# Optimization experiments

Measured on AMD Instinct MI355X. Metric: run time of the kernel, lower is better.

Reference implementation:

```python
import jax, jax.numpy as jnp
import numpy as np

N, T, D_MODEL, H, DK = 4, 4096, 1024, 16, 64


def setup_inputs() -> dict:
    key = jax.random.key(0)
    ks = jax.random.split(key, 16)
    randn = lambda k, sh: jax.random.normal(k, sh, dtype=jnp.float32)
    # linear weights stored (in, out) so y = x @ W + b (math-equivalent to torch Linear)
    scale = 1.0 / np.sqrt(D_MODEL)
    return {
        "x_k": randn(ks[0], (N, T, D_MODEL)),
        "x_v": randn(ks[1], (N, T, D_MODEL)),
        "x_q": randn(ks[2], (N, T, D_MODEL)),
        "mask": jnp.ones((N, T), dtype=jnp.int32),
        "Wk": randn(ks[3], (D_MODEL, H * DK)) * scale,
        "bk": randn(ks[4], (H * DK,)) * 0.02,
        "Wv": randn(ks[5], (D_MODEL, H * DK)) * scale,
        "bv": randn(ks[6], (H * DK,)) * 0.02,
        "Wq": randn(ks[7], (D_MODEL, H * DK)) * scale,
        "bq": randn(ks[8], (H * DK,)) * 0.02,
        "alpha_w": randn(ks[9], (DK,)),
        "beta_w": randn(ks[10], (DK,)),
        "Wr": randn(ks[11], (DK, DK)) * (1.0 / np.sqrt(DK)),
        "br": randn(ks[12], (DK,)) * 0.02,
        "Wfc": randn(ks[13], (H * DK, D_MODEL)) * scale,
        "bfc": randn(ks[14], (D_MODEL,)) * 0.02,
    }


def _split_heads(x):  # (n, t, h*d) -> (n, h, t, d)
    n, t, _ = x.shape
    return x.reshape(n, t, H, DK).transpose(0, 2, 1, 3)


def reference(x_k, x_v, x_q, mask, Wk, bk, Wv, bv, Wq, bq,
              alpha_w, beta_w, Wr, br, Wfc, bfc):
    scale = DK ** (-0.5)
    k = _split_heads(x_k @ Wk + bk)  # (n, h, t, d)
    v = _split_heads(x_v @ Wv + bv)
    q = _split_heads(x_q @ Wq + bq)

    m = (mask == 0)[:, None, :]  # (n, 1, t) True where masked
    neg_inf = jnp.finfo(q.dtype).min

    # alpha pooling over queries -> global query (n, h, d)
    alpha = jnp.einsum('nhtd,d->nht', q, alpha_w) * scale
    alpha = jnp.where(m, neg_inf, alpha)
    alpha = jax.nn.softmax(alpha, axis=-1)
    global_query = jnp.einsum('nht,nhtd->nhd', alpha, q)

    # p = broadcast(global_query) * k, then beta pooling -> global key
    p = global_query[:, :, None, :] * k  # (n, h, t, d)
    beta = jnp.einsum('nhtd,d->nht', p, beta_w) * scale
    beta = jnp.where(m, neg_inf, beta)
    beta = jax.nn.softmax(beta, axis=-1)
    global_key = jnp.einsum('nht,nhtd->nhd', beta, p)

    u = global_key[:, :, None, :] * v  # (n, h, t, d)
    u_r = u @ Wr + br
    A = u_r + q  # (n, h, t, d)
    A = A.transpose(0, 2, 1, 3).reshape(N, T, H * DK)
    return A @ Wfc + bfc
```

## Files before the change

### kernel.cpp

```cpp
#include <hip/hip_runtime.h>

typedef __bf16 bf16x8 __attribute__((ext_vector_type(8)));
typedef float f32x4 __attribute__((ext_vector_type(4)));
typedef unsigned int u32x4 __attribute__((ext_vector_type(4)));
typedef unsigned short u16x4 __attribute__((ext_vector_type(4)));
typedef unsigned short u16x8 __attribute__((ext_vector_type(8)));

#define SEQ_T 4096
#define DMODEL 1024
#define HEADS 16
#define DKH 64
#define MTOK 16384

#define AS1 __attribute__((address_space(1)))
#define AS3 __attribute__((address_space(3)))

__device__ __forceinline__ unsigned short f2bf(float f) {
  unsigned u = __builtin_bit_cast(unsigned int, f);
  u += 0x7FFFu + ((u >> 16) & 1u);
  return (unsigned short)(u >> 16);
}
__device__ __forceinline__ float bf2f(unsigned short h) {
  unsigned u = ((unsigned)h) << 16;
  return __builtin_bit_cast(float, u);
}
__device__ __forceinline__ void gload16(const unsigned short* g, unsigned short* l) {
  __builtin_amdgcn_global_load_lds((const AS1 unsigned int*)(g),
                                   (AS3 unsigned int*)(l), 16, 0, 0);
}

__device__ __forceinline__ void cvt_block(const float* __restrict__ x,
                                          unsigned short* __restrict__ y,
                                          size_t b, int tid) {
  f32x4 a0 = *(const f32x4*)(x + b + tid * 4);
  f32x4 a1 = *(const f32x4*)(x + b + 1024 + tid * 4);
  u16x4 o0, o1;
#pragma unroll
  for (int j = 0; j < 4; ++j) {
    o0[j] = f2bf(a0[j]);
    o1[j] = f2bf(a1[j]);
  }
  *(u16x4*)(y + b + tid * 4) = o0;
  *(u16x4*)(y + b + 1024 + tid * 4) = o1;
}

__global__ void __launch_bounds__(256) k_cvt(const float* __restrict__ x,
                                             unsigned short* __restrict__ y) {
  cvt_block(x, y, (size_t)blockIdx.x * 2048, threadIdx.x);
}

__global__ void __launch_bounds__(256) k_cvt3(const float* __restrict__ xq,
                                              const float* __restrict__ xk,
                                              const float* __restrict__ xv,
                                              unsigned short* __restrict__ oq,
                                              unsigned short* __restrict__ ok,
                                              unsigned short* __restrict__ ov) {
  const int which = blockIdx.x >> 13;
  const float* x = which == 0 ? xq : (which == 1 ? xk : xv);
  unsigned short* y = which == 0 ? oq : (which == 1 ? ok : ov);
  cvt_block(x, y, (size_t)(blockIdx.x & 8191) * 2048, threadIdx.x);
}

__global__ void __launch_bounds__(256) k_wtrans(const float* __restrict__ W,
                                                unsigned short* __restrict__ Wt,
                                                int K, int N) {
  __shared__ float tile[32][33];
  int bn = blockIdx.x * 32, bk = blockIdx.y * 32;
  int tx = threadIdx.x, ty = threadIdx.y;
#pragma unroll
  for (int j = 0; j < 32; j += 8)
    tile[ty + j][tx] = W[(size_t)(bk + ty + j) * N + bn + tx];
  __syncthreads();
#pragma unroll
  for (int j = 0; j < 32; j += 8)
    Wt[(size_t)(bn + ty + j) * K + bk + tx] = f2bf(tile[tx][ty + j]);
}

#define BM 128
#define BN 128
#define BK 64

template <int OBF, int SCORE, int FUSEA>
__global__ void __launch_bounds__(256, 2)
k_gemm(const unsigned short* __restrict__ A, const unsigned short* __restrict__ Bt,
       const float* __restrict__ bias, void* __restrict__ C,
       const int* __restrict__ mask, const float* __restrict__ swt,
       float* __restrict__ sbuf, const unsigned short* __restrict__ qadd,
       int M, int N, int K) {
  __shared__ unsigned short As[BM * BK];
  __shared__ unsigned short Bs[BN * BK];
  const int tid = threadIdx.x;
  const int lane = tid & 63, wid = tid >> 6;
  const int wr = wid >> 1, wc = wid & 1;
  const int l15 = lane & 15, l4 = lane >> 4;

  const int nwg = gridDim.x * gridDim.y;
  const int flat = blockIdx.x + blockIdx.y * gridDim.x;
  const int rm = (flat & 7) * (nwg >> 3) + (flat >> 3);
  const int bx = rm % gridDim.x, by = rm / gridDim.x;
  const int bm = by * BM, bn = bx * BN;

  const unsigned short* Btn = FUSEA ? Bt + ((size_t)(bm >> 12) << 20) : Bt;
  const float* biasn = FUSEA ? bias + ((bm >> 12) << 10) : bias;

  f32x4 acc[4][4];
#pragma unroll
  for (int i = 0; i < 4; ++i)
#pragma unroll
    for (int j = 0; j < 4; ++j)
#pragma unroll
      for (int e = 0; e < 4; ++e) acc[i][j][e] = 0.f;

  const int sgr = lane >> 3;
  const int sgc = (lane & 7) ^ sgr;

  for (int kt = 0; kt < K; kt += BK) {
    __syncthreads();
#pragma unroll
    for (int j = 0; j < 4; ++j) {
      int rb = wid * 32 + j * 8;
      gload16(A + (size_t)(bm + rb + sgr) * K + kt + sgc * 8, As + rb * BK);
    }
#pragma unroll
    for (int j = 0; j < 4; ++j) {
      int rb = wid * 32 + j * 8;
      gload16(Btn + (size_t)(bn + rb + sgr) * K + kt + sgc * 8, Bs + rb * BK);
    }
    __syncthreads();
#pragma unroll
    for (int kh = 0; kh < 2; ++kh) {
      bf16x8 af[4], bfr[4];
#pragma unroll
      for (int m = 0; m < 4; ++m) {
        int ra = wr * 64 + m * 16 + l15;
        int sl = (kh * 4 + l4) ^ (ra & 7);
        af[m] = *(const bf16x8*)(As + ra * BK + sl * 8);
      }
#pragma unroll
      for (int n = 0; n < 4; ++n) {
        int rb = wc * 64 + n * 16 + l15;
        int sl = (kh * 4 + l4) ^ (rb & 7);
        bfr[n] = *(const bf16x8*)(Bs + rb * BK + sl * 8);
      }
#pragma unroll
      for (int m = 0; m < 4; ++m)
#pragma unroll
        for (int n = 0; n < 4; ++n)
          acc[m][n] = __builtin_amdgcn_mfma_f32_16x16x32_bf16(af[m], bfr[n],
                                                              acc[m][n], 0, 0, 0);
    }
  }

  const int crow = bm + wr * 64 + l4 * 4;
  const int ccol = bn + wc * 64 + l15;

  float pacc[4][4];
  const float* wrow = nullptr;
  if (SCORE == 1) wrow = swt;
  if (SCORE) {
#pragma unroll
    for (int m = 0; m < 4; ++m)
#pragma unroll
      for (int e = 0; e < 4; ++e) pacc[m][e] = 0.f;
  }

#pragma unroll
  for (int m = 0; m < 4; ++m)
#pragma unroll
    for (int n = 0; n < 4; ++n) {
      int c = ccol + n * 16;
      float bj = biasn[c];
      float wg = SCORE ? wrow[n * 16 + l15] : 0.f;
#pragma unroll
      for (int e = 0; e < 4; ++e) {
        int r = crow + m * 16 + e;
        float v = acc[m][n][e] + bj;
        if (FUSEA) v += bf2f(qadd[(size_t)r * N + c]);
        if (SCORE) pacc[m][e] += v * wg;
        if (OBF)
          ((unsigned short*)C)[(size_t)r * N + c] = f2bf(v);
        else
          ((float*)C)[(size_t)r * N + c] = v;
      }
    }

  if (SCORE) {
#pragma unroll
    for (int m = 0; m < 4; ++m)
#pragma unroll
      for (int e = 0; e < 4; ++e) {
        float p = pacc[m][e];
        p += __shfl_xor(p, 1);
        p += __shfl_xor(p, 2);
        p += __shfl_xor(p, 4);
        p += __shfl_xor(p, 8);
        if (l15 == 0) {
          int r = crow + m * 16 + e;
          int t = r & (SEQ_T - 1), n = r >> 12;
          float sc = p * 0.125f;
          if (mask[n * SEQ_T + t] == 0) sc = -3.0e38f;
          sbuf[((size_t)n * HEADS + bx * 2 + wc) * SEQ_T + t] = sc;
        }
      }
  }
}

__global__ void __launch_bounds__(256) k_softmax(const float* __restrict__ s,
                                                 float* __restrict__ mxo,
                                                 float* __restrict__ invo) {
  __shared__ float red[4];
  const int tid = threadIdx.x, lane = tid & 63, wid = tid >> 6;
  const float* sb = s + (size_t)blockIdx.x * SEQ_T;
  float m = -3.4e38f;
  for (int t = tid; t < SEQ_T; t += 256) m = fmaxf(m, sb[t]);
#pragma unroll
  for (int o = 1; o < 64; o <<= 1) m = fmaxf(m, __shfl_xor(m, o));
  if (lane == 0) red[wid] = m;
  __syncthreads();
  m = fmaxf(fmaxf(red[0], red[1]), fmaxf(red[2], red[3]));
  __syncthreads();
  float sum = 0.f;
  for (int t = tid; t < SEQ_T; t += 256) sum += __expf(sb[t] - m);
#pragma unroll
  for (int o = 1; o < 64; o <<= 1) sum += __shfl_xor(sum, o);
  if (lane == 0) red[wid] = sum;
  __syncthreads();
  if (tid == 0) {
    mxo[blockIdx.x] = m;
    invo[blockIdx.x] = 1.f / (red[0] + red[1] + red[2] + red[3]);
  }
}

__global__ void __launch_bounds__(256) k_wsum(const unsigned short* __restrict__ X,
                                              const float* __restrict__ s,
                                              const float* __restrict__ mxv,
                                              const float* __restrict__ invv,
                                              float* __restrict__ pbuf) {
  __shared__ float part[16][64];
  const int nh = blockIdx.x >> 4, chunk = blockIdx.x & 15;
  const int n = nh >> 4, h = nh & 15;
  const int tid = threadIdx.x, lane = tid & 63, wid = tid >> 6;
  const int tsub = lane >> 4, dl = lane & 15;
  const float mx = mxv[nh], inv = invv[nh];
  const float* sb = s + (size_t)nh * SEQ_T + chunk * 256;
  const size_t base = ((size_t)n * SEQ_T + chunk * 256) * DMODEL + h * DKH + dl * 4;
  f32x4 acc = {0.f, 0.f, 0.f, 0.f};
  for (int t = wid * 4 + tsub; t < 256; t += 16) {
    float w = __expf(sb[t] - mx) * inv;
    u16x4 xv = *(const u16x4*)(X + base + (size_t)t * DMODEL);
    acc[0] += w * bf2f(xv[0]);
    acc[1] += w * bf2f(xv[1]);
    acc[2] += w * bf2f(xv[2]);
    acc[3] += w * bf2f(xv[3]);
  }
  int g = wid * 4 + tsub;
#pragma unroll
  for (int e = 0; e < 4; ++e) part[g][dl * 4 + e] = acc[e];
  __syncthreads();
  if (tid < 64) {
    float v = 0.f;
#pragma unroll
    for (int gg = 0; gg < 16; ++gg) v += part[gg][tid];
    pbuf[(size_t)blockIdx.x * 64 + tid] = v;
  }
}

__global__ void __launch_bounds__(256) k_wksb(const float* __restrict__ Wk,
                                              const float* __restrict__ bk,
                                              const float* __restrict__ pbuf,
                                              const float* __restrict__ bw,
                                              float* __restrict__ gq,
                                              unsigned short* __restrict__ WksT,
                                              float* __restrict__ bks) {
  const int nh = blockIdx.x, tid = threadIdx.x;
  const int n = nh >> 4, h = nh & 15;
  __shared__ float wvs[64];
  if (tid < 64) {
    float v = 0.f;
#pragma unroll
    for (int c = 0; c < 16; ++c) v += pbuf[((size_t)nh * 16 + c) * 64 + tid];
    gq[(size_t)nh * 64 + tid] = v;
    wvs[tid] = v * bw[tid];
  }
  __syncthreads();
  int c0 = tid * 4;
  u16x4 o;
#pragma unroll
  for (int i = 0; i < 4; ++i) {
    int c = c0 + i;
    const float* wr = Wk + (size_t)c * DMODEL + h * DKH;
    float acc = 0.f;
#pragma unroll
    for (int dd = 0; dd < 64; dd += 4) {
      f32x4 w4 = *(const f32x4*)(wr + dd);
      acc += w4[0] * wvs[dd] + w4[1] * wvs[dd + 1] + w4[2] * wvs[dd + 2] +
             w4[3] * wvs[dd + 3];
    }
    o[i] = f2bf(acc);
  }
  *(u16x4*)(WksT + (size_t)n * 16 * DMODEL + (size_t)h * DMODEL + c0) = o;
  if (tid < 64) {
    float p = bk[h * 64 + tid] * wvs[tid];
#pragma unroll
    for (int ofs = 1; ofs < 64; ofs <<= 1) p += __shfl_xor(p, ofs);
    if (tid == 0) bks[nh] = p;
  }
}

__global__ void __launch_bounds__(128) k_score(const unsigned short* __restrict__ xk,
                                               const unsigned short* __restrict__ WksT,
                                               const float* __restrict__ bks,
                                               const int* __restrict__ mask,
                                               float* __restrict__ sbuf) {
  __shared__ unsigned short Xs[64 * 32];
  __shared__ unsigned short Ws[16 * 32];
  const int tid = threadIdx.x, lane = tid & 63, wid = tid >> 6;
  const int l15 = lane & 15, l4 = lane >> 4;
  const int bm = blockIdx.x * 64;
  const int n = bm >> 12;
  const unsigned short* Wn = WksT + (size_t)n * 16 * DMODEL;

  f32x4 acc[2];
#pragma unroll
  for (int m = 0; m < 2; ++m)
#pragma unroll
    for (int e = 0; e < 4; ++e) acc[m][e] = 0.f;

  const int srow = lane >> 2, scol = (lane & 3) * 8;
  for (int kt = 0; kt < DMODEL; kt += 32) {
    __syncthreads();
#pragma unroll
    for (int j = 0; j < 2; ++j) {
      int rb = wid * 32 + j * 16;
      gload16(xk + (size_t)(bm + rb + srow) * DMODEL + kt + scol, Xs + rb * 32);
    }
    if (wid == 0) gload16(Wn + (size_t)srow * DMODEL + kt + scol, Ws);
    __syncthreads();
    bf16x8 bfr = *(const bf16x8*)(Ws + l15 * 32 + l4 * 8);
#pragma unroll
    for (int m = 0; m < 2; ++m) {
      bf16x8 af = *(const bf16x8*)(Xs + (wid * 32 + m * 16 + l15) * 32 + l4 * 8);
      acc[m] = __builtin_amdgcn_mfma_f32_16x16x32_bf16(af, bfr, acc[m], 0, 0, 0);
    }
  }
  const int h = l15;
  const float bh = bks[n * 16 + h];
#pragma unroll
  for (int m = 0; m < 2; ++m)
#pragma unroll
    for (int e = 0; e < 4; ++e) {
      int r = bm + wid * 32 + m * 16 + l4 * 4 + e;
      int t = r & (SEQ_T - 1);
      float sc = (acc[m][e] + bh) * 0.125f;
      if (mask[n * SEQ_T + t] == 0) sc = -3.0e38f;
      sbuf[((size_t)n * HEADS + h) * SEQ_T + t] = sc;
    }
}

__global__ void __launch_bounds__(256) k_bwsum(const unsigned short* __restrict__ xk,
                                               const float* __restrict__ s,
                                               const float* __restrict__ smx,
                                               const float* __restrict__ sinv,
                                               float* __restrict__ part) {
  __shared__ float eb[16][64];
  const int tc = blockIdx.x, n = blockIdx.y, tid = threadIdx.x;
#pragma unroll
  for (int i = 0; i < 4; ++i) {
    int idx = i * 256 + tid;
    int h = idx >> 6, t = idx & 63;
    int nh = n * 16 + h;
    eb[h][t] = __expf(s[(size_t)nh * SEQ_T + tc * 64 + t] - smx[nh]) * sinv[nh];
  }
  __syncthreads();
  const int c0 = tid * 4;
  f32x4 acc[16];
#pragma unroll
  for (int h = 0; h < 16; ++h)
#pragma unroll
    for (int e = 0; e < 4; ++e) acc[h][e] = 0.f;
  const unsigned short* xb = xk + ((size_t)n * SEQ_T + tc * 64) * DMODEL + c0;
  for (int t = 0; t < 64; ++t) {
    u16x4 xr = *(const u16x4*)(xb + (size_t)t * DMODEL);
    float x0 = bf2f(xr[0]), x1 = bf2f(xr[1]), x2 = bf2f(xr[2]), x3 = bf2f(xr[3]);
#pragma unroll
    for (int h = 0; h < 16; ++h) {
      float w = eb[h][t];
      acc[h][0] += w * x0;
      acc[h][1] += w * x1;
      acc[h][2] += w * x2;
      acc[h][3] += w * x3;
    }
  }
#pragma unroll
  for (int h = 0; h < 16; ++h)
    *(f32x4*)(part + (((size_t)(n * 64 + tc)) * 16 + h) * DMODEL + c0) = acc[h];
}

__global__ void __launch_bounds__(256) k_gkrw(const float* __restrict__ part,
                                              const unsigned short* __restrict__ WkT,
                                              const float* __restrict__ bk,
                                              const float* __restrict__ gq,
                                              const float* __restrict__ Wr,
                                              const float* __restrict__ bv,
                                              const float* __restrict__ br,
                                              unsigned short* __restrict__ WrgT,
                                              float* __restrict__ bcomb) {
  __shared__ float pl[DMODEL];
  __shared__ float gks[64];
  __shared__ float wl[4096];
  const int nh = blockIdx.x, tid = threadIdx.x;
  const int n = nh >> 4, h = nh & 15;
  const int c0 = tid * 4;
  f32x4 a4 = {0.f, 0.f, 0.f, 0.f};
  for (int tc = 0; tc < 64; ++tc) {
    f32x4 p = *(const f32x4*)(part + (((size_t)(n * 64 + tc)) * 16 + h) * DMODEL + c0);
    a4[0] += p[0]; a4[1] += p[1]; a4[2] += p[2]; a4[3] += p[3];
  }
#pragma unroll
  for (int e = 0; e < 4; ++e) pl[c0 + e] = a4[e];
  __syncthreads();
  if (tid < 64) {
    const unsigned short* wr = WkT + (size_t)(h * 64 + tid) * DMODEL;
    float acc = 0.f;
    for (int c = 0; c < DMODEL; c += 8) {
      u16x8 w = *(const u16x8*)(wr + c);
#pragma unroll
      for (int j = 0; j < 8; ++j) acc += pl[c + j] * bf2f(w[j]);
    }
    gks[tid] = gq[(size_t)nh * 64 + tid] * (acc + bk[h * 64 + tid]);
  }
  __syncthreads();
#pragma unroll
  for (int i = 0; i < 16; ++i) {
    int idx = i * 256 + tid;
    int d = idx >> 6, dd = idx & 63;
    float v = gks[dd] * Wr[dd * 64 + d];
    wl[idx] = v;
    WrgT[(size_t)nh * 4096 + idx] = f2bf(v);
  }
  __syncthreads();
  if (tid < 64) {
    float acc = br[tid];
#pragma unroll
    for (int dd = 0; dd < 64; ++dd) acc += bv[h * 64 + dd] * wl[tid * 64 + dd];
    bcomb[(size_t)n * DMODEL + h * 64 + tid] = acc;
  }
}

#define LDW 72
__global__ void __launch_bounds__(256) k_wcomb(const unsigned short* __restrict__ WrgT,
                                               const unsigned short* __restrict__ WvN,
                                               unsigned short* __restrict__ WcombT) {
  __shared__ unsigned short Wg[64 * LDW];
  __shared__ unsigned short Vv[128 * LDW];
  const int rc = blockIdx.x, nh = blockIdx.y;
  const int n = nh >> 4, h = nh & 15;
  const int tid = threadIdx.x, lane = tid & 63, wid = tid >> 6;
  const int l15 = lane & 15, l4 = lane >> 4;
#pragma unroll
  for (int i = 0; i < 2; ++i) {
    int v = i * 256 + tid;
    int d = v >> 3, k8 = v & 7;
    *(u16x8*)(Wg + d * LDW + k8 * 8) =
        *(const u16x8*)(WrgT + (size_t)nh * 4096 + d * 64 + k8 * 8);
  }
#pragma unroll
  for (int i = 0; i < 4; ++i) {
    int v = i * 256 + tid;
    int r = v >> 3, k8 = v & 7;
    *(u16x8*)(Vv + r * LDW + k8 * 8) =
        *(const u16x8*)(WvN + (size_t)(rc * 128 + r) * DMODEL + h * 64 + k8 * 8);
  }
  __syncthreads();
  f32x4 acc[8];
#pragma unroll
  for (int ct = 0; ct < 8; ++ct)
#pragma unroll
    for (int e = 0; e < 4; ++e) acc[ct][e] = 0.f;
#pragma unroll
  for (int ks = 0; ks < 2; ++ks) {
    bf16x8 af = *(const bf16x8*)(Wg + (wid * 16 + l15) * LDW + ks * 32 + l4 * 8);
#pragma unroll
    for (int ct = 0; ct < 8; ++ct) {
      bf16x8 bf = *(const bf16x8*)(Vv + (ct * 16 + l15) * LDW + ks * 32 + l4 * 8);
      acc[ct] = __builtin_amdgcn_mfma_f32_16x16x32_bf16(af, bf, acc[ct], 0, 0, 0);
    }
  }
  unsigned short* out = WcombT + ((size_t)n << 20);
#pragma unroll
  for (int ct = 0; ct < 8; ++ct)
#pragma unroll
    for (int e = 0; e < 4; ++e) {
      int d = h * 64 + wid * 16 + l4 * 4 + e;
      int r = rc * 128 + ct * 16 + l15;
      out[(size_t)d * DMODEL + r] = f2bf(acc[ct][e]);
    }
}

extern "C" void kernel_launch(void* const* d_in, const int* in_sizes, int n_in,
                              void* d_out, int out_size, void* d_ws, size_t ws_size,
                              hipStream_t stream) {
  const float* x_k = (const float*)d_in[0];
  const float* x_v = (const float*)d_in[1];
  const float* x_q = (const float*)d_in[2];
  const int* mask = (const int*)d_in[3];
  const float* Wk = (const float*)d_in[4];
  const float* bk = (const float*)d_in[5];
  const float* Wv = (const float*)d_in[6];
  const float* bv = (const float*)d_in[7];
  const float* Wq = (const float*)d_in[8];
  const float* bq = (const float*)d_in[9];
  const float* alpha_w = (const float*)d_in[10];
  const float* beta_w = (const float*)d_in[11];
  const float* Wr = (const float*)d_in[12];
  const float* br = (const float*)d_in[13];
  const float* Wfc = (const float*)d_in[14];
  const float* bfc = (const float*)d_in[15];

  unsigned short* qbf = (unsigned short*)d_out;
  unsigned short* xvb = (unsigned short*)d_out + (size_t)MTOK * DMODEL;

  char* ws = (char*)d_ws;
  const size_t MB = 1024 * 1024;
  unsigned short* xst = (unsigned short*)(ws);
  unsigned short* abuf = (unsigned short*)(ws + 32 * MB);
  unsigned short* WqT = (unsigned short*)(ws + 64 * MB);
  unsigned short* WkT = WqT + (size_t)DMODEL * DMODEL;
  unsigned short* WfT = WkT + (size_t)DMODEL * DMODEL;
  unsigned short* WvN = WfT + (size_t)DMODEL * DMODEL;
  unsigned short* WcombT = WvN + (size_t)DMODEL * DMODEL;
  unsigned short* WrgT = WcombT + (size_t)4 * DMODEL * DMODEL;
  unsigned short* WksT = WrgT + (size_t)64 * 4096;
  float* part = (float*)(WksT + (size_t)4 * 16 * DMODEL);
  float* sbuf = part + (size_t)256 * 16 * DMODEL;
  float* pbuf = sbuf + (size_t)64 * SEQ_T;
  float* smx = pbuf + 1024 * 64;
  float* sinv = smx + 64;
  float* gq = sinv + 64;
  float* bks = gq + 4096;
  float* bcomb = bks + 64;

  dim3 tb(32, 8);
  dim3 tg(DMODEL / 32, DMODEL / 32);
  k_wtrans<<<tg, tb, 0, stream>>>(Wq, WqT, DMODEL, DMODEL);
  k_wtrans<<<tg, tb, 0, stream>>>(Wk, WkT, DMODEL, DMODEL);
  k_wtrans<<<tg, tb, 0, stream>>>(Wfc, WfT, DMODEL, DMODEL);
  k_cvt<<<512, 256, 0, stream>>>(Wv, WvN);

  k_cvt3<<<3 * 8192, 256, 0, stream>>>(x_q, x_k, x_v, xst, abuf, xvb);

  dim3 ggrid(DMODEL / BN, MTOK / BM);

  k_gemm<1, 1, 0><<<ggrid, 256, 0, stream>>>(xst, WqT, bq, (void*)qbf, mask,
                                             alpha_w, sbuf, nullptr,
                                             MTOK, DMODEL, DMODEL);
  k_softmax<<<64, 256, 0, stream>>>(sbuf, smx, sinv);
  k_wsum<<<1024, 256, 0, stream>>>(qbf, sbuf, smx, sinv, pbuf);
  k_wksb<<<64, 256, 0, stream>>>(Wk, bk, pbuf, beta_w, gq, WksT, bks);

  k_score<<<MTOK / 64, 128, 0, stream>>>(abuf, WksT, bks, mask, sbuf);
  k_softmax<<<64, 256, 0, stream>>>(sbuf, smx, sinv);
  dim3 bwg(64, 4);
  k_bwsum<<<bwg, 256, 0, stream>>>(abuf, sbuf, smx, sinv, part);
  k_gkrw<<<64, 256, 0, stream>>>(part, WkT, bk, gq, Wr, bv, br, WrgT, bcomb);

  dim3 wcg(8, 64);
  k_wcomb<<<wcg, 256, 0, stream>>>(WrgT, WvN, WcombT);

  k_gemm<1, 0, 1><<<ggrid, 256, 0, stream>>>(xvb, WcombT, bcomb, (void*)abuf,
                                             nullptr, nullptr, nullptr, qbf,
                                             MTOK, DMODEL, DMODEL);

  k_gemm<0, 0, 0><<<ggrid, 256, 0, stream>>>(abuf, WfT, bfc, d_out, nullptr,
                                             nullptr, nullptr, nullptr,
                                             MTOK, DMODEL, DMODEL);
}
```

Baseline: 271.2 us.

## Double-buffer GEMM LDS tiles and use nontemporal accesses in conversion

The GEMM main loop now ping-pongs between two LDS buffers, issuing the global-to-LDS loads for the next K tile before computing on the current one, with one barrier per iteration instead of two. This aims to overlap memory latency with MFMA work. LDS use doubles to 64KB per block, which may limit the two-blocks-per-CU occupancy target. The fp32-to-bf16 conversion kernel also switches to nontemporal loads and stores to reduce cache pollution.

Measured after the change: 303.8 us. 1.12x slower.

```diff
diff --git a/kernel.cpp b/kernel.cpp
--- a/kernel.cpp
+++ b/kernel.cpp
@@ -32,16 +32,16 @@
 __device__ __forceinline__ void cvt_block(const float* __restrict__ x,
                                           unsigned short* __restrict__ y,
                                           size_t b, int tid) {
-  f32x4 a0 = *(const f32x4*)(x + b + tid * 4);
-  f32x4 a1 = *(const f32x4*)(x + b + 1024 + tid * 4);
+  f32x4 a0 = __builtin_nontemporal_load((const f32x4*)(x + b + tid * 4));
+  f32x4 a1 = __builtin_nontemporal_load((const f32x4*)(x + b + 1024 + tid * 4));
   u16x4 o0, o1;
 #pragma unroll
   for (int j = 0; j < 4; ++j) {
     o0[j] = f2bf(a0[j]);
     o1[j] = f2bf(a1[j]);
   }
-  *(u16x4*)(y + b + tid * 4) = o0;
-  *(u16x4*)(y + b + 1024 + tid * 4) = o1;
+  __builtin_nontemporal_store(o0, (u16x4*)(y + b + tid * 4));
+  __builtin_nontemporal_store(o1, (u16x4*)(y + b + 1024 + tid * 4));
 }
 
 __global__ void __launch_bounds__(256) k_cvt(const float* __restrict__ x,
@@ -87,8 +87,8 @@
        const int* __restrict__ mask, const float* __restrict__ swt,
        float* __restrict__ sbuf, const unsigned short* __restrict__ qadd,
        int M, int N, int K) {
-  __shared__ unsigned short As[BM * BK];
-  __shared__ unsigned short Bs[BN * BK];
+  __shared__ unsigned short As[2 * BM * BK];
+  __shared__ unsigned short Bs[2 * BN * BK];
   const int tid = threadIdx.x;
   const int lane = tid & 63, wid = tid >> 6;
   const int wr = wid >> 1, wc = wid & 1;
@@ -113,20 +113,30 @@
 
   const int sgr = lane >> 3;
   const int sgc = (lane & 7) ^ sgr;
-
-  for (int kt = 0; kt < K; kt += BK) {
-    __syncthreads();
+  const int nt = K / BK;
+
+  auto stage = [&](int t) {
+    unsigned short* Ad = As + (t & 1) * (BM * BK);
+    unsigned short* Bd = Bs + (t & 1) * (BN * BK);
 #pragma unroll
     for (int j = 0; j < 4; ++j) {
       int rb = wid * 32 + j * 8;
-      gload16(A + (size_t)(bm + rb + sgr) * K + kt + sgc * 8, As + rb * BK);
+      gload16(A + (size_t)(bm + rb + sgr) * K + t * BK + sgc * 8, Ad + rb * BK);
     }
 #pragma unroll
     for (int j = 0; j < 4; ++j) {
       int rb = wid * 32 + j * 8;
-      gload16(Btn + (size_t)(bn + rb + sgr) * K + kt + sgc * 8, Bs + rb * BK);
-    }
-    __syncthreads();
+      gload16(Btn + (size_t)(bn + rb + sgr) * K + t * BK + sgc * 8, Bd + rb * BK);
+    }
+  };
+
+  stage(0);
+  __syncthreads();
+
+  for (int t = 0; t < nt; ++t) {
+    if (t + 1 < nt) stage(t + 1);
+    const unsigned short* Ab = As + (t & 1) * (BM * BK);
+    const unsigned short* Bb = Bs + (t & 1) * (BN * BK);
 #pragma unroll
     for (int kh = 0; kh < 2; ++kh) {
       bf16x8 af[4], bfr[4];
@@ -134,13 +144,13 @@
       for (int m = 0; m < 4; ++m) {
         int ra = wr * 64 + m * 16 + l15;
         int sl = (kh * 4 + l4) ^ (ra & 7);
-        af[m] = *(const bf16x8*)(As + ra * BK + sl * 8);
+        af[m] = *(const bf16x8*)(Ab + ra * BK + sl * 8);
       }
 #pragma unroll
       for (int n = 0; n < 4; ++n) {
         int rb = wc * 64 + n * 16 + l15;
         int sl = (kh * 4 + l4) ^ (rb & 7);
-        bfr[n] = *(const bf16x8*)(Bs + rb * BK + sl * 8);
+        bfr[n] = *(const bf16x8*)(Bb + rb * BK + sl * 8);
       }
 #pragma unroll
       for (int m = 0; m < 4; ++m)
@@ -149,6 +159,7 @@
           acc[m][n] = __builtin_amdgcn_mfma_f32_16x16x32_bf16(af[m], bfr[n],
                                                               acc[m][n], 0, 0, 0);
     }
+    __syncthreads();
   }
 
   const int crow = bm + wr * 64 + l4 * 4;
```
